# Kernel optimization log

Measured on AMD Instinct MI355X. Metric: run time of the kernel, lower is better.

The kernel has to match this reference:

```python
import jax, jax.numpy as jnp
import numpy as np

N, QLEN, KLEN = 4, 2048, 2048
QDIM = KVDIM = 512
EMBED, HEADS = 1024, 16
HEAD_DIM = EMBED // HEADS


def setup_inputs() -> dict:
    key = jax.random.key(0)
    ks = jax.random.split(key, 7)
    return {
        "queries": jax.random.normal(ks[0], (N, QLEN, QDIM), dtype=jnp.float32),
        "keys": jax.random.normal(ks[1], (1, KLEN, KVDIM), dtype=jnp.float32),
        "values": jax.random.normal(ks[2], (1, KLEN, KVDIM), dtype=jnp.float32),
        "mask": jax.random.randint(ks[3], (N, 1, 1, KLEN), 0, 2, dtype=jnp.int32),
        "Wq": jax.random.normal(ks[4], (QDIM, EMBED), dtype=jnp.float32) * (QDIM ** -0.5),
        "Wk": jax.random.normal(ks[5], (KVDIM, EMBED), dtype=jnp.float32) * (KVDIM ** -0.5),
        "Wv": jax.random.normal(ks[6], (KVDIM, EMBED), dtype=jnp.float32) * (KVDIM ** -0.5),
    }


def reference(queries, keys, values, mask, Wq, Wk, Wv):
    # Projections (Linear, no bias)
    q = (queries @ Wq).reshape(N, QLEN, HEADS, HEAD_DIM)      # [N, Q, H, D]
    k = (keys @ Wk).reshape(KLEN, HEADS, HEAD_DIM)            # [K, H, D] (batch-1, shared)
    v = (values @ Wv).reshape(KLEN, HEADS, HEAD_DIM)          # [K, H, D]

    # energy: [N, H, Q, K]
    energy = jnp.einsum('nqhd,khd->nhqk', q, k)
    energy = jnp.where(mask == 0, jnp.float32(-1e20), energy)
    attn = jax.nn.softmax(energy / jnp.float32(HEAD_DIM ** 0.5), axis=3)

    out = jnp.einsum('nhqk,khd->nqhd', attn, v)               # [N, Q, H, D]
    return out.reshape(N, QLEN, EMBED)
```

## Files before the change

kernel.cpp:

```cpp
#include <hip/hip_runtime.h>

#define NB 4
#define QLEN 2048
#define KLEN 2048
#define QDIM 512
#define EMBED 1024
#define HEADS 16
#define HD 64

typedef __bf16 bf16x8 __attribute__((ext_vector_type(8)));
typedef float f32x2 __attribute__((ext_vector_type(2)));
typedef float f32x4 __attribute__((ext_vector_type(4)));
typedef float f32x16 __attribute__((ext_vector_type(16)));

#define CLOG 0.18033688011112042f

__device__ __forceinline__ float fexp2(float x) {
#if __has_builtin(__builtin_amdgcn_exp2f)
    return __builtin_amdgcn_exp2f(x);
#else
    float r;
    asm("v_exp_f32 %0, %1\n\ts_nop 1" : "=v"(r) : "v"(x));
    return r;
#endif
}

#if __has_builtin(__builtin_amdgcn_sched_barrier)
#define SCHED_FENCE() __builtin_amdgcn_sched_barrier(0)
#else
#define SCHED_FENCE()
#endif

__device__ __forceinline__ void dma16(const void* g, void* l) {
    __builtin_amdgcn_global_load_lds(
        (const __attribute__((address_space(1))) void*)g,
        (__attribute__((address_space(3))) void*)l, 16, 0, 0);
}

__global__ __launch_bounds__(256) void prep(const float* __restrict__ q,
                                            const float* __restrict__ k,
                                            const float* __restrict__ v,
                                            const float* __restrict__ Wq,
                                            const float* __restrict__ Wk,
                                            const float* __restrict__ Wv,
                                            const int* __restrict__ mask,
                                            __bf16* __restrict__ qd,
                                            __bf16* __restrict__ kd,
                                            __bf16* __restrict__ vd,
                                            __bf16* __restrict__ WtQ,
                                            __bf16* __restrict__ WtK,
                                            __bf16* __restrict__ WtV,
                                            int* __restrict__ pidx,
                                            int* __restrict__ cntg,
                                            __bf16* __restrict__ kbf,
                                            __bf16* __restrict__ vtbf,
                                            int* __restrict__ cidx,
                                            int* __restrict__ pst) {
    __shared__ float tile[32][33];
    __shared__ int part[256];
    int b = blockIdx.x, tid = threadIdx.x;
    if (b >= 4612) {
        int t2 = b - 4612, n = t2 >> 4, h = t2 & 15;
        const int* mp = mask + n * KLEN + tid * 8;
        int4 ma = *(const int4*)&mp[0];
        int4 mb = *(const int4*)&mp[4];
        int c = (ma.x != 0) + (ma.y != 0) + (ma.z != 0) + (ma.w != 0)
              + (mb.x != 0) + (mb.y != 0) + (mb.z != 0) + (mb.w != 0);
        part[tid] = c;
        __syncthreads();
        for (int off = 128; off > 0; off >>= 1) {
            if (tid < off) part[tid] += part[tid + off];
            __syncthreads();
        }
        int cnt = part[0];
        int tiles = (cnt + 63) >> 6, pe = tiles << 6, np = pe - cnt;
        __bf16* kb0 = kbf + (((size_t)(n * HEADS + h)) * KLEN + cnt) * HD;
        __bf16* vb0 = vtbf + ((size_t)(n * HEADS + h)) * HD * KLEN;
        for (int i = tid; i < np * HD; i += 256) {
            int r = i >> 6, d = i & 63;
            kb0[r * HD + d] = (__bf16)0.f;
        }
        for (int d = 0; d < HD; d++)
            if (tid < np) vb0[(size_t)d * KLEN + cnt + tid] = (__bf16)0.f;
    } else if (b >= 4608) {
        int n = b - 4608;
        const int* mp = mask + n * KLEN + tid * 8;
        int4 ma = *(const int4*)&mp[0];
        int4 mb = *(const int4*)&mp[4];
        int m[8] = { ma.x, ma.y, ma.z, ma.w, mb.x, mb.y, mb.z, mb.w };
        int c = 0;
#pragma unroll
        for (int j = 0; j < 8; j++) c += (m[j] != 0);
        part[tid] = c;
        __syncthreads();
        for (int off = 1; off < 256; off <<= 1) {
            int vv = (tid >= off) ? part[tid - off] : 0;
            __syncthreads();
            part[tid] += vv;
            __syncthreads();
        }
        int pos = part[tid] - c;
        int* pw = pidx + n * KLEN + tid * 8;
        int* cw = cidx + n * KLEN;
#pragma unroll
        for (int j = 0; j < 8; j++) {
            pw[j] = m[j] ? pos : -1;
            if (m[j]) cw[pos] = tid * 8 + j;
            pos += (m[j] != 0);
        }
        if ((tid & 15) == 0) pst[n * 17 + (tid >> 4)] = part[tid] - c;
        if (tid == 255) pst[n * 17 + 16] = part[255];
        if (tid == 0) cntg[n] = part[255];
    } else if (b < 3072) {
        const float* src; __bf16* dst; int cb;
        if (b < 2048)      { src = q; dst = qd; cb = b; }
        else if (b < 2560) { src = k; dst = kd; cb = b - 2048; }
        else               { src = v; dst = vd; cb = b - 2560; }
        int i = (cb * 256 + tid) * 8;
        float4 a0 = *(const float4*)&src[i];
        float4 a1 = *(const float4*)&src[i + 4];
        bf16x8 o;
        o[0] = (__bf16)a0.x; o[1] = (__bf16)a0.y; o[2] = (__bf16)a0.z; o[3] = (__bf16)a0.w;
        o[4] = (__bf16)a1.x; o[5] = (__bf16)a1.y; o[6] = (__bf16)a1.z; o[7] = (__bf16)a1.w;
        *(bf16x8*)&dst[i] = o;
    } else {
        int tb = b - 3072;
        int which = tb >> 9, r = tb & 511;
        const float* src = (which == 0) ? Wq : (which == 1) ? Wk : Wv;
        __bf16* dst = (which == 0) ? WtQ : (which == 1) ? WtK : WtV;
        float scale = (which == 0) ? CLOG : 1.0f;
        int e0 = (r & 31) * 32, c0 = (r >> 5) * 32;
        int tx = tid & 31, ty = tid >> 5;
        for (int i = 0; i < 4; i++)
            tile[ty + 8 * i][tx] = src[(c0 + ty + 8 * i) * EMBED + e0 + tx];
        __syncthreads();
        for (int i = 0; i < 4; i++)
            dst[(e0 + ty + 8 * i) * QDIM + c0 + tx] = (__bf16)(tile[tx][ty + 8 * i] * scale);
    }
}

__device__ __forceinline__ void gemm_compute(const __bf16* As, const __bf16* Bs,
                                             int wr, int wc, int r16, int qq,
                                             f32x4 (&acc)[4][4]) {
    bf16x8 af[4], bq[4];
#pragma unroll
    for (int i = 0; i < 4; i++)
        af[i] = *(const bf16x8*)&As[(wr * 64 + i * 16 + r16) * 32 + qq * 8];
#pragma unroll
    for (int j = 0; j < 4; j++)
        bq[j] = *(const bf16x8*)&Bs[(wc * 64 + j * 16 + r16) * 32 + qq * 8];
#pragma unroll
    for (int i = 0; i < 4; i++)
#pragma unroll
        for (int j = 0; j < 4; j++)
            acc[i][j] = __builtin_amdgcn_mfma_f32_16x16x32_bf16(af[i], bq[j], acc[i][j], 0, 0, 0);
}

__device__ __forceinline__ void gemm128(const __bf16* __restrict__ A,
                                        const __bf16* __restrict__ Bt,
                                        __bf16* As0, __bf16* As1,
                                        __bf16* Bs0, __bf16* Bs1,
                                        int row0, int col0, f32x4 (&acc)[4][4]) {
    int tid = threadIdx.x, wave = tid >> 6, lane = tid & 63;
    int r16 = lane & 15, qq = lane >> 4;
    int wr = wave >> 1, wc = wave & 1;
    const __bf16* agp1 = A + (size_t)(row0 + (tid >> 2)) * QDIM + (tid & 3) * 8;
    const __bf16* agp2 = A + (size_t)(row0 + 64 + (tid >> 2)) * QDIM + (tid & 3) * 8;
    const __bf16* bgp1 = Bt + (size_t)(col0 + (tid >> 2)) * QDIM + (tid & 3) * 8;
    const __bf16* bgp2 = Bt + (size_t)(col0 + 64 + (tid >> 2)) * QDIM + (tid & 3) * 8;
    __bf16 *a0a = &As0[wave * 512], *a0b = &As0[2048 + wave * 512];
    __bf16 *a1a = &As1[wave * 512], *a1b = &As1[2048 + wave * 512];
    __bf16 *b0a = &Bs0[wave * 512], *b0b = &Bs0[2048 + wave * 512];
    __bf16 *b1a = &Bs1[wave * 512], *b1b = &Bs1[2048 + wave * 512];

    dma16(agp1, a0a); dma16(agp2, a0b);
    dma16(bgp1, b0a); dma16(bgp2, b0b);
    agp1 += 32; agp2 += 32; bgp1 += 32; bgp2 += 32;
    __syncthreads();

    for (int t = 0; t < 16; t += 2) {
        dma16(agp1, a1a); dma16(agp2, a1b);
        dma16(bgp1, b1a); dma16(bgp2, b1b);
        agp1 += 32; agp2 += 32; bgp1 += 32; bgp2 += 32;
        SCHED_FENCE();
        gemm_compute(As0, Bs0, wr, wc, r16, qq, acc);
        __syncthreads();
        if (t + 2 < 16) {
            dma16(agp1, a0a); dma16(agp2, a0b);
            dma16(bgp1, b0a); dma16(bgp2, b0b);
            agp1 += 32; agp2 += 32; bgp1 += 32; bgp2 += 32;
        }
        SCHED_FENCE();
        gemm_compute(As1, Bs1, wr, wc, r16, qq, acc);
        __syncthreads();
    }
}

__global__ __launch_bounds__(256) void proj_all(const __bf16* __restrict__ qin,
                                                const __bf16* __restrict__ kin,
                                                const __bf16* __restrict__ vin,
                                                const __bf16* __restrict__ wtq,
                                                const __bf16* __restrict__ wtk,
                                                const __bf16* __restrict__ wtv,
                                                const int* __restrict__ pidx,
                                                const int* __restrict__ cidx,
                                                const int* __restrict__ pst,
                                                __bf16* __restrict__ qout,
                                                __bf16* __restrict__ kout,
                                                __bf16* __restrict__ vtout) {
    __shared__ __align__(16) __bf16 smem[16384];
    int bid = blockIdx.x;
    const __bf16 *A, *Bt;
    int mode, b, row0, col0;
    if (bid < 128)      { A = wtv; Bt = vin; mode = 2; b = bid;
                          row0 = (b >> 4) * 128; col0 = (b & 15) * 128; }
    else if (bid < 256) { A = kin; Bt = wtk; mode = 1; b = bid - 128;
                          row0 = (b >> 3) * 128; col0 = (b & 7) * 128; }
    else                { A = qin; Bt = wtq; mode = 0; b = bid - 256;
                          row0 = (b >> 3) * 128; col0 = (b & 7) * 128; }
    f32x4 acc[4][4] = {};
    gemm128(A, Bt, smem, smem + 4096, smem + 8192, smem + 12288, row0, col0, acc);
    int tid = threadIdx.x;
    int lane = tid & 63, wave = tid >> 6;
    int r16 = lane & 15, qq = lane >> 4;
    int wr = wave >> 1, wc = wave & 1;

    if (mode == 0) {
#pragma unroll
        for (int i = 0; i < 4; i++)
#pragma unroll
            for (int j = 0; j < 4; j++)
#pragma unroll
                for (int rr = 0; rr < 4; rr++) {
                    int grow = row0 + wr * 64 + i * 16 + qq * 4 + rr;
                    int gcol = col0 + wc * 64 + j * 16 + r16;
                    int hh = gcol >> 6, d = gcol & 63;
                    int n = grow >> 11, qr = grow & 2047;
                    qout[((size_t)(n * HEADS + hh) * QLEN + qr) * HD + d] =
                        (__bf16)acc[i][j][rr];
                }
    } else if (mode == 1) {
#pragma unroll
        for (int i = 0; i < 4; i++) {
            int grow0 = row0 + wr * 64 + i * 16 + qq * 4;
            int4 p4[NB];
#pragma unroll
            for (int nn = 0; nn < NB; nn++)
                p4[nn] = *(const int4*)&pidx[nn * KLEN + grow0];
#pragma unroll
            for (int j = 0; j < 4; j++) {
                int gcol = col0 + wc * 64 + j * 16 + r16;
                int hh = gcol >> 6, d = gcol & 63;
#pragma unroll
                for (int rr = 0; rr < 4; rr++) {
                    __bf16 v = (__bf16)acc[i][j][rr];
#pragma unroll
                    for (int nn = 0; nn < NB; nn++) {
                        int p = ((const int*)&p4[nn])[rr];
                        if (p >= 0)
                            kout[((size_t)(nn * HEADS + hh) * KLEN + p) * HD + d] = v;
                    }
                }
            }
        }
    } else {
        __bf16* Ct = smem;
#pragma unroll
        for (int i = 0; i < 4; i++)
#pragma unroll
            for (int j = 0; j < 4; j++)
#pragma unroll
                for (int rr = 0; rr < 4; rr++) {
                    int row = wr * 64 + i * 16 + qq * 4 + rr;
                    int colx = wc * 64 + j * 16 + r16;
                    Ct[row * 128 + colx] = (__bf16)acc[i][j][rr];
                }
        __syncthreads();
        int ci0 = col0 >> 7;
        for (int nn = 0; nn < NB; nn++) {
            int pstart = pst[nn * 17 + ci0];
            int pend   = pst[nn * 17 + ci0 + 1];
            int cv = pend - pstart;
            if (cv <= 0) continue;
            const int* cix = cidx + nn * KLEN;
            __bf16* vbase = vtout + (size_t)(nn * EMBED + row0) * KLEN;
            int p0a = (pstart + 7) & ~7;
            int p1a = pend & ~7;
            int headEnd = min(p0a, pend);
            int nh = headEnd - pstart;
            if (nh > 0) {
                int r = tid & 7;
                if (r < nh) {
                    int p = pstart + r;
                    int kk = cix[p] - col0;
                    for (int e = tid >> 3; e < 128; e += 32)
                        vbase[(size_t)e * KLEN + p] = Ct[e * 128 + kk];
                }
            }
            if (p1a > p0a) {
                int nch = (p1a - p0a) >> 3;
                for (int ch = tid & 31; ch < nch; ch += 32) {
                    int p = p0a + ch * 8;
                    int4 ca = *(const int4*)&cix[p];
                    int4 cb = *(const int4*)&cix[p + 4];
                    int k0 = ca.x - col0, k1 = ca.y - col0, k2 = ca.z - col0, k3 = ca.w - col0;
                    int k4 = cb.x - col0, k5 = cb.y - col0, k6 = cb.z - col0, k7 = cb.w - col0;
                    for (int e = tid >> 5; e < 128; e += 8) {
                        const __bf16* cr = &Ct[e * 128];
                        bf16x8 o;
                        o[0] = cr[k0]; o[1] = cr[k1]; o[2] = cr[k2]; o[3] = cr[k3];
                        o[4] = cr[k4]; o[5] = cr[k5]; o[6] = cr[k6]; o[7] = cr[k7];
                        *(bf16x8*)&vbase[(size_t)e * KLEN + p] = o;
                    }
                }
            }
            int t0 = max(p1a, headEnd);
            int nt = pend - t0;
            if (nt > 0) {
                int r = tid & 7;
                if (r < nt) {
                    int p = t0 + r;
                    int kk = cix[p] - col0;
                    for (int e = tid >> 3; e < 128; e += 32)
                        vbase[(size_t)e * KLEN + p] = Ct[e * 128 + kk];
                }
            }
        }
    }
}

__device__ __forceinline__ void attn_tile(const __bf16* ksb, const __bf16* vsb,
                                          const bf16x8 (&qfrag)[4],
                                          int col, int h,
                                          f32x16& o0, f32x16& o1, f32x2& rsl) {
    bf16x8 pfrag[4];
#pragma unroll
    for (int kt2 = 0; kt2 < 2; kt2++) {
        int R = kt2 * 32 + col;
        f32x16 s = {};
        __builtin_amdgcn_s_setprio(1);
#pragma unroll
        for (int c = 0; c < 4; c++) {
            int cc = (2 * c + h) ^ (R & 7);
            bf16x8 kf = *(const bf16x8*)&ksb[(R * 8 + cc) * 8];
            s = __builtin_amdgcn_mfma_f32_32x32x16_bf16(kf, qfrag[c], s, 0, 0, 0);
        }
        __builtin_amdgcn_s_setprio(0);
#pragma unroll
        for (int G = 0; G < 4; G++) {
            int ci = 2 * kt2 + (G >> 1), e0 = (G & 1) * 4;
#pragma unroll
            for (int rr = 0; rr < 4; rr += 2) {
                float p0 = fexp2(s[4 * G + rr]);
                float p1 = fexp2(s[4 * G + rr + 1]);
                f32x2 pp; pp[0] = p0; pp[1] = p1;
                rsl += pp;
                pfrag[ci][e0 + rr] = (__bf16)p0;
                pfrag[ci][e0 + rr + 1] = (__bf16)p1;
            }
        }
    }
    __builtin_amdgcn_s_setprio(1);
#pragma unroll
    for (int c = 0; c < 4; c++) {
        int cc = (2 * c + h) ^ (col & 7);
        bf16x8 v0 = *(const bf16x8*)&vsb[(col * 8 + cc) * 8];
        bf16x8 v1 = *(const bf16x8*)&vsb[((32 + col) * 8 + cc) * 8];
        o0 = __builtin_amdgcn_mfma_f32_32x32x16_bf16(v0, pfrag[c], o0, 0, 0, 0);
        o1 = __builtin_amdgcn_mfma_f32_32x32x16_bf16(v1, pfrag[c], o1, 0, 0, 0);
    }
    __builtin_amdgcn_s_setprio(0);
}

__global__ __launch_bounds__(256, 4) void attn_kernel(const __bf16* __restrict__ qb,
                                                      const __bf16* __restrict__ kb,
                                                      const __bf16* __restrict__ vtb,
                                                      const int* __restrict__ cntg,
                                                      float* __restrict__ out) {
    __shared__ __align__(16) __bf16 ks[2][4096];
    __shared__ __align__(16) __bf16 vs[2][4096];

    int tid = threadIdx.x, wave = tid >> 6, lane = tid & 63;
    int col = lane & 31, h = lane >> 5;
    int bid = blockIdx.x;
    int qx = bid >> 6, r6 = bid & 63, hh = r6 >> 2, n = r6 & 3;
    int q0 = qx * 128;
    int cnt = cntg[n];
    int tiles = (cnt + 63) >> 6;
    int npad = (tiles << 6) - cnt;
    const __bf16* qg = qb + ((size_t)(n * HEADS + hh) * QLEN + q0 + wave * 32 + col) * HD;
    const __bf16* kg = kb + (size_t)(n * HEADS + hh) * KLEN * HD;
    const __bf16* vg = vtb + (size_t)(n * HEADS + hh) * HD * KLEN;

    bf16x8 qfrag[4];
#pragma unroll
    for (int c = 0; c < 4; c++) qfrag[c] = *(const bf16x8*)&qg[c * 16 + h * 8];

    int s1 = tid, R1 = s1 >> 3, c1 = (s1 & 7) ^ (R1 & 7);
    int s2 = tid + 256, R2 = s2 >> 3, c2 = (s2 & 7) ^ (R2 & 7);
    int g1 = (R1 & 0x33) | ((R1 & 4) << 1) | ((R1 & 8) >> 1);
    int g2 = (R2 & 0x33) | ((R2 & 4) << 1) | ((R2 & 8) >> 1);
    const __bf16* kgp1 = kg + g1 * HD + c1 * 8;
    const __bf16* kgp2 = kg + g2 * HD + c2 * 8;
    const __bf16* vgp1 = vg + (size_t)R1 * KLEN + c1 * 8;
    const __bf16* vgp2 = vg + (size_t)R2 * KLEN + c2 * 8;
    __bf16 *kl0a = &ks[0][wave * 512], *kl0b = &ks[0][2048 + wave * 512];
    __bf16 *kl1a = &ks[1][wave * 512], *kl1b = &ks[1][2048 + wave * 512];
    __bf16 *vl0a = &vs[0][wave * 512], *vl0b = &vs[0][2048 + wave * 512];
    __bf16 *vl1a = &vs[1][wave * 512], *vl1b = &vs[1][2048 + wave * 512];

    dma16(kgp1, kl0a); dma16(kgp2, kl0b);
    dma16(vgp1, vl0a); dma16(vgp2, vl0b);
    kgp1 += 64 * HD; kgp2 += 64 * HD; vgp1 += 64; vgp2 += 64;
    __syncthreads();

    f32x16 o0 = {}, o1 = {};
    f32x2 rsl = {};

    for (int t = 0; t < tiles; t++) {
        int pc = t & 1;
        if (t + 1 < tiles) {
            if (pc) { dma16(kgp1, kl0a); dma16(kgp2, kl0b);
                      dma16(vgp1, vl0a); dma16(vgp2, vl0b); }
            else    { dma16(kgp1, kl1a); dma16(kgp2, kl1b);
                      dma16(vgp1, vl1a); dma16(vgp2, vl1b); }
            kgp1 += 64 * HD; kgp2 += 64 * HD; vgp1 += 64; vgp2 += 64;
        }
        SCHED_FENCE();
        attn_tile(ks[pc], vs[pc], qfrag, col, h, o0, o1, rsl);
        __syncthreads();
    }

    float rs = rsl[0] + rsl[1];
    rs += __shfl_xor(rs, 32);
    rs -= (float)npad;
    float inv = 1.0f / rs;
    float* op = out + ((size_t)n * QLEN + q0 + wave * 32 + col) * EMBED + hh * HD;
#pragma unroll
    for (int G = 0; G < 4; G++) {
        float4 t0, t1;
        t0.x = o0[4 * G + 0] * inv; t0.y = o0[4 * G + 1] * inv;
        t0.z = o0[4 * G + 2] * inv; t0.w = o0[4 * G + 3] * inv;
        t1.x = o1[4 * G + 0] * inv; t1.y = o1[4 * G + 1] * inv;
        t1.z = o1[4 * G + 2] * inv; t1.w = o1[4 * G + 3] * inv;
        *(float4*)&op[8 * G + 4 * h] = t0;
        *(float4*)&op[32 + 8 * G + 4 * h] = t1;
    }
}

extern "C" void kernel_launch(void* const* d_in, const int* in_sizes, int n_in,
                              void* d_out, int out_size, void* d_ws, size_t ws_size,
                              hipStream_t stream) {
    const float* queries = (const float*)d_in[0];
    const float* keys    = (const float*)d_in[1];
    const float* values  = (const float*)d_in[2];
    const int*   mask    = (const int*)d_in[3];
    const float* Wq      = (const float*)d_in[4];
    const float* Wk      = (const float*)d_in[5];
    const float* Wv      = (const float*)d_in[6];
    float* out = (float*)d_out;

    const size_t MiB = 1048576;
    char* ws = (char*)d_ws;
    __bf16* qbf   = (__bf16*)(ws);
    __bf16* kbf   = (__bf16*)(ws + 16 * MiB);
    __bf16* vtbf  = (__bf16*)(ws + 32 * MiB);
    __bf16* wtq   = (__bf16*)(ws + 48 * MiB);
    __bf16* wtk   = (__bf16*)(ws + 49 * MiB);
    __bf16* wtv   = (__bf16*)(ws + 50 * MiB);
    __bf16* qin   = (__bf16*)(ws + 51 * MiB);
    __bf16* kin   = (__bf16*)(ws + 59 * MiB);
    __bf16* vin   = (__bf16*)(ws + 61 * MiB);
    int*    pidx  = (int*)(ws + 63 * MiB);
    int*    cntg  = (int*)(ws + 63 * MiB + 65536);
    int*    cidx  = (int*)(ws + 63 * MiB + 131072);
    int*    pst   = (int*)(ws + 63 * MiB + 196608);

    prep<<<4676, 256, 0, stream>>>(queries, keys, values, Wq, Wk, Wv, mask,
                                   qin, kin, vin, wtq, wtk, wtv,
                                   pidx, cntg, kbf, vtbf, cidx, pst);
    proj_all<<<768, 256, 0, stream>>>(qin, kin, vin, wtq, wtk, wtv,
                                      pidx, cidx, pst, qbf, kbf, vtbf);
    attn_kernel<<<1024, 256, 0, stream>>>(qbf, kbf, vtbf, cntg, out);
}
```

Measured before the change: 162.3 us.

## Fuse Q projection into attention kernel prologue, drop Q from proj_all

Each attention block now computes its own 128x64 Q tile (queries @ Wq for one head) with an MFMA GEMM in shared memory, then loads the Q fragments from LDS instead of reading a precomputed Q buffer. proj_all now only handles the K and V projections, with 256 blocks instead of 768. This removes the Q write and re-read through global memory and shrinks the projection launch. The cost is a longer attention prologue and a reused 32KB shared buffer; the attention blocks' Q GEMM is not redundant since each (n, q-tile, head) is unique.

```diff
diff --git a/kernel.cpp b/kernel.cpp
--- a/kernel.cpp
+++ b/kernel.cpp
@@ -196,16 +196,13 @@
     }
 }
 
-__global__ __launch_bounds__(256) void proj_all(const __bf16* __restrict__ qin,
-                                                const __bf16* __restrict__ kin,
+__global__ __launch_bounds__(256) void proj_all(const __bf16* __restrict__ kin,
                                                 const __bf16* __restrict__ vin,
-                                                const __bf16* __restrict__ wtq,
                                                 const __bf16* __restrict__ wtk,
                                                 const __bf16* __restrict__ wtv,
                                                 const int* __restrict__ pidx,
                                                 const int* __restrict__ cidx,
                                                 const int* __restrict__ pst,
-                                                __bf16* __restrict__ qout,
                                                 __bf16* __restrict__ kout,
                                                 __bf16* __restrict__ vtout) {
     __shared__ __align__(16) __bf16 smem[16384];
@@ -214,9 +211,7 @@
     int mode, b, row0, col0;
     if (bid < 128)      { A = wtv; Bt = vin; mode = 2; b = bid;
                           row0 = (b >> 4) * 128; col0 = (b & 15) * 128; }
-    else if (bid < 256) { A = kin; Bt = wtk; mode = 1; b = bid - 128;
-                          row0 = (b >> 3) * 128; col0 = (b & 7) * 128; }
-    else                { A = qin; Bt = wtq; mode = 0; b = bid - 256;
+    else                { A = kin; Bt = wtk; mode = 1; b = bid - 128;
                           row0 = (b >> 3) * 128; col0 = (b & 7) * 128; }
     f32x4 acc[4][4] = {};
     gemm128(A, Bt, smem, smem + 4096, smem + 8192, smem + 12288, row0, col0, acc);
@@ -225,21 +220,7 @@
     int r16 = lane & 15, qq = lane >> 4;
     int wr = wave >> 1, wc = wave & 1;
 
-    if (mode == 0) {
-#pragma unroll
-        for (int i = 0; i < 4; i++)
-#pragma unroll
-            for (int j = 0; j < 4; j++)
-#pragma unroll
-                for (int rr = 0; rr < 4; rr++) {
-                    int grow = row0 + wr * 64 + i * 16 + qq * 4 + rr;
-                    int gcol = col0 + wc * 64 + j * 16 + r16;
-                    int hh = gcol >> 6, d = gcol & 63;
-                    int n = grow >> 11, qr = grow & 2047;
-                    qout[((size_t)(n * HEADS + hh) * QLEN + qr) * HD + d] =
-                        (__bf16)acc[i][j][rr];
-                }
-    } else if (mode == 1) {
+    if (mode == 1) {
 #pragma unroll
         for (int i = 0; i < 4; i++) {
             int grow0 = row0 + wr * 64 + i * 16 + qq * 4;
@@ -372,13 +353,13 @@
     __builtin_amdgcn_s_setprio(0);
 }
 
-__global__ __launch_bounds__(256, 4) void attn_kernel(const __bf16* __restrict__ qb,
+__global__ __launch_bounds__(256, 4) void attn_kernel(const __bf16* __restrict__ qin,
+                                                      const __bf16* __restrict__ wtq,
                                                       const __bf16* __restrict__ kb,
                                                       const __bf16* __restrict__ vtb,
                                                       const int* __restrict__ cntg,
                                                       float* __restrict__ out) {
-    __shared__ __align__(16) __bf16 ks[2][4096];
-    __shared__ __align__(16) __bf16 vs[2][4096];
+    __shared__ __align__(16) __bf16 smem[16384];
 
     int tid = threadIdx.x, wave = tid >> 6, lane = tid & 63;
     int col = lane & 31, h = lane >> 5;
@@ -388,13 +369,89 @@
     int cnt = cntg[n];
     int tiles = (cnt + 63) >> 6;
     int npad = (tiles << 6) - cnt;
-    const __bf16* qg = qb + ((size_t)(n * HEADS + hh) * QLEN + q0 + wave * 32 + col) * HD;
     const __bf16* kg = kb + (size_t)(n * HEADS + hh) * KLEN * HD;
     const __bf16* vg = vtb + (size_t)(n * HEADS + hh) * HD * KLEN;
 
     bf16x8 qfrag[4];
-#pragma unroll
-    for (int c = 0; c < 4; c++) qfrag[c] = *(const bf16x8*)&qg[c * 16 + h * 8];
+    {
+        const __bf16* A  = qin + (size_t)(n * QLEN + q0) * QDIM;
+        const __bf16* Bt = wtq + (size_t)(hh * HD) * QDIM;
+        int r16 = lane & 15, qq = lane >> 4;
+        int wr = wave >> 1, wc = wave & 1;
+        f32x4 acc[4][2] = {};
+        const __bf16* agp1 = A + (size_t)(tid >> 2) * QDIM + (tid & 3) * 8;
+        const __bf16* agp2 = agp1 + (size_t)64 * QDIM;
+        const __bf16* bgp  = Bt + (size_t)(tid >> 2) * QDIM + (tid & 3) * 8;
+        __bf16 *a0a = &smem[wave * 512],        *a0b = &smem[2048 + wave * 512];
+        __bf16 *a1a = &smem[4096 + wave * 512], *a1b = &smem[6144 + wave * 512];
+        __bf16 *b0  = &smem[8192 + wave * 512], *b1  = &smem[10240 + wave * 512];
+
+        dma16(agp1, a0a); dma16(agp2, a0b); dma16(bgp, b0);
+        agp1 += 32; agp2 += 32; bgp += 32;
+        __syncthreads();
+
+        for (int t = 0; t < 16; t += 2) {
+            dma16(agp1, a1a); dma16(agp2, a1b); dma16(bgp, b1);
+            agp1 += 32; agp2 += 32; bgp += 32;
+            SCHED_FENCE();
+            {
+                bf16x8 af[4], bq[2];
+#pragma unroll
+                for (int i = 0; i < 4; i++)
+                    af[i] = *(const bf16x8*)&smem[(wr * 64 + i * 16 + r16) * 32 + qq * 8];
+#pragma unroll
+                for (int j = 0; j < 2; j++)
+                    bq[j] = *(const bf16x8*)&smem[8192 + (wc * 32 + j * 16 + r16) * 32 + qq * 8];
+#pragma unroll
+                for (int i = 0; i < 4; i++)
+#pragma unroll
+                    for (int j = 0; j < 2; j++)
+                        acc[i][j] = __builtin_amdgcn_mfma_f32_16x16x32_bf16(af[i], bq[j], acc[i][j], 0, 0, 0);
+            }
+            __syncthreads();
+            if (t + 2 < 16) {
+                dma16(agp1, a0a); dma16(agp2, a0b); dma16(bgp, b0);
+                agp1 += 32; agp2 += 32; bgp += 32;
+            }
+            SCHED_FENCE();
+            {
+                bf16x8 af[4], bq[2];
+#pragma unroll
+                for (int i = 0; i < 4; i++)
+                    af[i] = *(const bf16x8*)&smem[4096 + (wr * 64 + i * 16 + r16) * 32 + qq * 8];
+#pragma unroll
+                for (int j = 0; j < 2; j++)
+                    bq[j] = *(const bf16x8*)&smem[10240 + (wc * 32 + j * 16 + r16) * 32 + qq * 8];
+#pragma unroll
+                for (int i = 0; i < 4; i++)
+#pragma unroll
+                    for (int j = 0; j < 2; j++)
+                        acc[i][j] = __builtin_amdgcn_mfma_f32_16x16x32_bf16(af[i], bq[j], acc[i][j], 0, 0, 0);
+            }
+            __syncthreads();
+        }
+
+#pragma unroll
+        for (int i = 0; i < 4; i++)
+#pragma unroll
+            for (int j = 0; j < 2; j++)
+#pragma unroll
+                for (int rr = 0; rr < 4; rr++) {
+                    int row = wr * 64 + i * 16 + qq * 4 + rr;
+                    int d   = wc * 32 + j * 16 + r16;
+                    smem[row * 64 + d] = (__bf16)acc[i][j][rr];
+                }
+        __syncthreads();
+#pragma unroll
+        for (int c = 0; c < 4; c++)
+            qfrag[c] = *(const bf16x8*)&smem[(wave * 32 + col) * 64 + c * 16 + h * 8];
+        __syncthreads();
+    }
+
+    __bf16* ks0 = smem;
+    __bf16* ks1 = smem + 4096;
+    __bf16* vs0 = smem + 8192;
+    __bf16* vs1 = smem + 12288;
 
     int s1 = tid, R1 = s1 >> 3, c1 = (s1 & 7) ^ (R1 & 7);
     int s2 = tid + 256, R2 = s2 >> 3, c2 = (s2 & 7) ^ (R2 & 7);
@@ -404,10 +461,10 @@
     const __bf16* kgp2 = kg + g2 * HD + c2 * 8;
     const __bf16* vgp1 = vg + (size_t)R1 * KLEN + c1 * 8;
     const __bf16* vgp2 = vg + (size_t)R2 * KLEN + c2 * 8;
-    __bf16 *kl0a = &ks[0][wave * 512], *kl0b = &ks[0][2048 + wave * 512];
-    __bf16 *kl1a = &ks[1][wave * 512], *kl1b = &ks[1][2048 + wave * 512];
-    __bf16 *vl0a = &vs[0][wave * 512], *vl0b = &vs[0][2048 + wave * 512];
-    __bf16 *vl1a = &vs[1][wave * 512], *vl1b = &vs[1][2048 + wave * 512];
+    __bf16 *kl0a = &ks0[wave * 512], *kl0b = &ks0[2048 + wave * 512];
+    __bf16 *kl1a = &ks1[wave * 512], *kl1b = &ks1[2048 + wave * 512];
+    __bf16 *vl0a = &vs0[wave * 512], *vl0b = &vs0[2048 + wave * 512];
+    __bf16 *vl1a = &vs1[wave * 512], *vl1b = &vs1[2048 + wave * 512];
 
     dma16(kgp1, kl0a); dma16(kgp2, kl0b);
     dma16(vgp1, vl0a); dma16(vgp2, vl0b);
@@ -427,7 +484,7 @@
             kgp1 += 64 * HD; kgp2 += 64 * HD; vgp1 += 64; vgp2 += 64;
         }
         SCHED_FENCE();
-        attn_tile(ks[pc], vs[pc], qfrag, col, h, o0, o1, rsl);
+        attn_tile(pc ? ks1 : ks0, pc ? vs1 : vs0, qfrag, col, h, o0, o1, rsl);
         __syncthreads();
     }
 
@@ -462,7 +519,6 @@
 
     const size_t MiB = 1048576;
     char* ws = (char*)d_ws;
-    __bf16* qbf   = (__bf16*)(ws);
     __bf16* kbf   = (__bf16*)(ws + 16 * MiB);
     __bf16* vtbf  = (__bf16*)(ws + 32 * MiB);
     __bf16* wtq   = (__bf16*)(ws + 48 * MiB);
@@ -479,7 +535,7 @@
     prep<<<4676, 256, 0, stream>>>(queries, keys, values, Wq, Wk, Wv, mask,
                                    qin, kin, vin, wtq, wtk, wtv,
                                    pidx, cntg, kbf, vtbf, cidx, pst);
-    proj_all<<<768, 256, 0, stream>>>(qin, kin, vin, wtq, wtk, wtv,
-                                      pidx, cidx, pst, qbf, kbf, vtbf);
-    attn_kernel<<<1024, 256, 0, stream>>>(qbf, kbf, vtbf, cntg, out);
-}
+    proj_all<<<256, 256, 0, stream>>>(kin, vin, wtk, wtv,
+                                      pidx, cidx, pst, kbf, vtbf);
+    attn_kernel<<<1024, 256, 0, stream>>>(qin, wtq, kbf, vtbf, cntg, out);
+}
```

Measured after the change: 165.0 us. About the same (+1.7%).
